# Kernel tuning notes

Measured on AMD Instinct MI355X. Metric: run time of the kernel, lower is better.

Reference implementation:

```python
import jax, jax.numpy as jnp
import numpy as np

N, E, D, H = 50000, 800000, 128, 8
DK = D // H
SQRT_DK = float(np.sqrt(DK))
LN_EPS = 1e-5


def setup_inputs() -> dict:
    key = jax.random.key(0)
    ks = jax.random.split(key, 16)
    s = 0.02
    inp = {
        "x": jax.random.normal(ks[0], (N, D), jnp.float32),
        "edge_index": jax.random.randint(ks[1], (2, E), 0, N, jnp.int32),
        "Wq": jax.random.normal(ks[2], (D, D), jnp.float32) * s,
        "bq": jnp.zeros((D,), jnp.float32),
        "Wk": jax.random.normal(ks[3], (D, D), jnp.float32) * s,
        "bk": jnp.zeros((D,), jnp.float32),
        "Wv": jax.random.normal(ks[4], (D, D), jnp.float32) * s,
        "bv": jnp.zeros((D,), jnp.float32),
        "ln_g": jnp.ones((D,), jnp.float32),
        "ln_b": jnp.zeros((D,), jnp.float32),
        "W1": jax.random.normal(ks[5], (D, 2 * D), jnp.float32) * s,
        "b1": jnp.zeros((2 * D,), jnp.float32),
        "W2": jax.random.normal(ks[6], (2 * D, D), jnp.float32) * s,
        "b2": jnp.zeros((D,), jnp.float32),
    }
    return inp


def _segment_softmax(scores, seg, num_segments):
    # scores: [E, H], seg: [E] target-node ids. Matches PyG softmax (1e-16 in denom).
    m = jax.ops.segment_max(scores, seg, num_segments=num_segments)
    ex = jnp.exp(scores - m[seg])
    den = jax.ops.segment_sum(ex, seg, num_segments=num_segments)
    return ex / (den[seg] + 1e-16)


def _forward(x, edge_index, Wq, bq, Wk, bk, Wv, bv, ln_g, ln_b, W1, b1, W2, b2):
    src, dst = edge_index[0], edge_index[1]
    n = x.shape[0]
    x_src = x[src]            # [E, D] gather
    x_dst = x[dst]            # [E, D] gather
    q = (x_dst @ Wq + bq).reshape(-1, H, DK)
    k = (x_src @ Wk + bk).reshape(-1, H, DK)
    v = (x_src @ Wv + bv).reshape(-1, H, DK)
    att = jnp.sum(q * k, axis=-1) / SQRT_DK          # [E, H]; edge_weight defaults to 1
    att = _segment_softmax(att, dst, n)              # segment softmax over dst
    msg = (v * att[..., None]).reshape(-1, D)        # [E, D]
    res = jax.ops.segment_sum(msg, dst, num_segments=n)  # scatter-add
    h = res + x
    # FFN with pre-LayerNorm, residual h + mlp(LN(h))
    mu = jnp.mean(h, axis=-1, keepdims=True)
    var = jnp.mean(jnp.square(h - mu), axis=-1, keepdims=True)
    hn = (h - mu) * jax.lax.rsqrt(var + LN_EPS) * ln_g + ln_b
    mlp = jax.nn.gelu(hn @ W1 + b1, approximate=False) @ W2 + b2
    return h + mlp


def reference(x, edge_index, Wq, bq, Wk, bk, Wv, bv, ln_g, ln_b, W1, b1, W2, b2):
    return _forward(x, edge_index, Wq, bq, Wk, bk, Wv, bv, ln_g, ln_b, W1, b1, W2, b2)
```

## Files before the change

kernel.cpp:

```cpp
#include <hip/hip_runtime.h>
#include <cmath>


typedef short v8s __attribute__((ext_vector_type(8)));
typedef float v4f __attribute__((ext_vector_type(4)));
typedef float v2f __attribute__((ext_vector_type(2)));

__device__ __forceinline__ float gelu_exact(float x) {
    return 0.5f * x * (1.0f + erff(x * 0.70710678118654752440f));
}

__device__ __forceinline__ unsigned short f2bf(float f) {
    unsigned int u = __float_as_uint(f);
    u = (u + 0x7fffu + ((u >> 16) & 1u)) >> 16;
    return (unsigned short)u;
}

__device__ __forceinline__ float2 bf2_to_f2(unsigned int u) {
    float2 r;
    r.x = __uint_as_float(u << 16);
    r.y = __uint_as_float(u & 0xffff0000u);
    return r;
}

__device__ __forceinline__ unsigned char f2fp8(float f) {
    unsigned int p = __builtin_amdgcn_cvt_pk_fp8_f32(f, f, 0, false);
    return (unsigned char)(p & 0xffu);
}

__device__ __forceinline__ void edge_accum(uint4 k4, uint4 v4, bool ok,
                                           const float2 (&qv)[8],
                                           float2 (&acc)[8], float& l) {
    v2f f;
    float d0 = 0.f, d1 = 0.f;
    f = __builtin_amdgcn_cvt_pk_f32_fp8(k4.x, false); d0 = fmaf(f[0], qv[0].x, fmaf(f[1], qv[0].y, d0));
    f = __builtin_amdgcn_cvt_pk_f32_fp8(k4.x, true);  d1 = fmaf(f[0], qv[1].x, fmaf(f[1], qv[1].y, d1));
    f = __builtin_amdgcn_cvt_pk_f32_fp8(k4.y, false); d0 = fmaf(f[0], qv[2].x, fmaf(f[1], qv[2].y, d0));
    f = __builtin_amdgcn_cvt_pk_f32_fp8(k4.y, true);  d1 = fmaf(f[0], qv[3].x, fmaf(f[1], qv[3].y, d1));
    f = __builtin_amdgcn_cvt_pk_f32_fp8(k4.z, false); d0 = fmaf(f[0], qv[4].x, fmaf(f[1], qv[4].y, d0));
    f = __builtin_amdgcn_cvt_pk_f32_fp8(k4.z, true);  d1 = fmaf(f[0], qv[5].x, fmaf(f[1], qv[5].y, d1));
    f = __builtin_amdgcn_cvt_pk_f32_fp8(k4.w, false); d0 = fmaf(f[0], qv[6].x, fmaf(f[1], qv[6].y, d0));
    f = __builtin_amdgcn_cvt_pk_f32_fp8(k4.w, true);  d1 = fmaf(f[0], qv[7].x, fmaf(f[1], qv[7].y, d1));
    float pe = ok ? __expf(d0 + d1) : 0.f;
    l += pe;
    f = __builtin_amdgcn_cvt_pk_f32_fp8(v4.x, false); acc[0].x = fmaf(pe, f[0], acc[0].x); acc[0].y = fmaf(pe, f[1], acc[0].y);
    f = __builtin_amdgcn_cvt_pk_f32_fp8(v4.x, true);  acc[1].x = fmaf(pe, f[0], acc[1].x); acc[1].y = fmaf(pe, f[1], acc[1].y);
    f = __builtin_amdgcn_cvt_pk_f32_fp8(v4.y, false); acc[2].x = fmaf(pe, f[0], acc[2].x); acc[2].y = fmaf(pe, f[1], acc[2].y);
    f = __builtin_amdgcn_cvt_pk_f32_fp8(v4.y, true);  acc[3].x = fmaf(pe, f[0], acc[3].x); acc[3].y = fmaf(pe, f[1], acc[3].y);
    f = __builtin_amdgcn_cvt_pk_f32_fp8(v4.z, false); acc[4].x = fmaf(pe, f[0], acc[4].x); acc[4].y = fmaf(pe, f[1], acc[4].y);
    f = __builtin_amdgcn_cvt_pk_f32_fp8(v4.z, true);  acc[5].x = fmaf(pe, f[0], acc[5].x); acc[5].y = fmaf(pe, f[1], acc[5].y);
    f = __builtin_amdgcn_cvt_pk_f32_fp8(v4.w, false); acc[6].x = fmaf(pe, f[0], acc[6].x); acc[6].y = fmaf(pe, f[1], acc[6].y);
    f = __builtin_amdgcn_cvt_pk_f32_fp8(v4.w, true);  acc[7].x = fmaf(pe, f[0], acc[7].x); acc[7].y = fmaf(pe, f[1], acc[7].y);
}


__global__ __launch_bounds__(256)
void prep_kernel(const float* __restrict__ Wq, const float* __restrict__ Wk,
                 const float* __restrict__ Wv, const float* __restrict__ W1,
                 const float* __restrict__ W2,
                 const float* __restrict__ bq, const float* __restrict__ bk,
                 const float* __restrict__ bv, const float* __restrict__ b1,
                 const float* __restrict__ b2,
                 unsigned short* __restrict__ wcat, unsigned short* __restrict__ w1t,
                 unsigned short* __restrict__ w2t, float* __restrict__ bcat) {
    int i = blockIdx.x * 256 + threadIdx.x;
    if (i < 49152) {
        int m = i >> 14, j = i & 16383;
        int c = j >> 7, k = j & 127;
        const float* W = (m == 0) ? Wq : (m == 1) ? Wk : Wv;
        wcat[i] = f2bf(W[k * 128 + c]);
    } else if (i < 49152 + 32768) {
        int j = i - 49152;
        int c = j >> 7, k = j & 127;
        w1t[j] = f2bf(W1[k * 256 + c]);
    } else if (i < 49152 + 65536) {
        int j = i - 49152 - 32768;
        int c = j >> 8, k = j & 255;
        w2t[j] = f2bf(W2[k * 128 + c]);
    } else if (i < 49152 + 65536 + 768) {
        int j = i - 49152 - 65536;
        float v;
        if (j < 128)      v = bq[j];
        else if (j < 256) v = bk[j - 128];
        else if (j < 384) v = bv[j - 256];
        else if (j < 640) v = b1[j - 384];
        else              v = b2[j - 640];
        bcat[j] = v;
    }
}


__global__ __launch_bounds__(256)
void scatter_kernel(const int* __restrict__ src, const int* __restrict__ dst,
                    int* __restrict__ cnt, int* __restrict__ slots, int E,
                    int nseg, int nbpr) {
    const int r = blockIdx.x & 7;
    const int b = blockIdx.x >> 3;
    const int lo = r * nseg, hi = lo + nseg;
    const int stride = nbpr * 256;
    const int E4 = E >> 2;
    for (int i = b * 256 + threadIdx.x; i < E4; i += stride) {
        int4 d4 = ((const int4*)dst)[i];
        int4 s4 = ((const int4*)src)[i];
        if (d4.x >= lo && d4.x < hi) { int p = atomicAdd(&cnt[d4.x], 1); if (p < 64) slots[(d4.x << 6) + p] = s4.x; }
        if (d4.y >= lo && d4.y < hi) { int p = atomicAdd(&cnt[d4.y], 1); if (p < 64) slots[(d4.y << 6) + p] = s4.y; }
        if (d4.z >= lo && d4.z < hi) { int p = atomicAdd(&cnt[d4.z], 1); if (p < 64) slots[(d4.z << 6) + p] = s4.z; }
        if (d4.w >= lo && d4.w < hi) { int p = atomicAdd(&cnt[d4.w], 1); if (p < 64) slots[(d4.w << 6) + p] = s4.w; }
    }
    if (b == 0) {
        for (int e = (E4 << 2) + threadIdx.x; e < E; e += 256) {
            int d = dst[e];
            if (d >= lo && d < hi) {
                int p = atomicAdd(&cnt[d], 1);
                if (p < 64) slots[(d << 6) + p] = src[e];
            }
        }
    }
}


__global__ __launch_bounds__(512)
void qkv_gemm_kernel(const float* __restrict__ A,
                     const unsigned short* __restrict__ wcat,
                     const float* __restrict__ bcat,
                     unsigned short* __restrict__ qb,
                     unsigned char* __restrict__ kvh,
                     int n_rows) {
    __shared__ unsigned short Xs[8192];

    const int t = threadIdx.x;
    const int l = t & 63;
    const int w = t >> 6;
    const int lq = l >> 4;
    const int lc = l & 15;
    const int rb = blockIdx.x * 64;

    #pragma unroll
    for (int it = 0; it < 2; ++it) {
        int idx = it * 512 + t;
        int row = idx >> 4, ch = idx & 15;
        v8s av = (v8s){0, 0, 0, 0, 0, 0, 0, 0};
        if (rb + row < n_rows) {
            const float* ap = &A[(size_t)(rb + row) * 128 + ch * 8];
            float4 f0 = *(const float4*)ap;
            float4 f1 = *(const float4*)(ap + 4);
            av[0] = (short)f2bf(f0.x); av[1] = (short)f2bf(f0.y);
            av[2] = (short)f2bf(f0.z); av[3] = (short)f2bf(f0.w);
            av[4] = (short)f2bf(f1.x); av[5] = (short)f2bf(f1.y);
            av[6] = (short)f2bf(f1.z); av[7] = (short)f2bf(f1.w);
        }
        *(v8s*)&Xs[row * 128 + ((ch ^ (row & 7)) * 8)] = av;
    }
    __syncthreads();

    v8s a[4][4];
    #pragma unroll
    for (int c = 0; c < 4; ++c)
        #pragma unroll
        for (int i = 0; i < 4; ++i)
            a[c][i] = *(const v8s*)&Xs[(i * 16 + lc) * 128 +
                                       (((c * 4 + lq) ^ (lc & 7)) * 8)];

    const int col = w * 16 + lc;
    #pragma unroll
    for (int y = 0; y < 3; ++y) {
        const unsigned short* Bt = wcat + y * 16384;
        v8s bf[4];
        #pragma unroll
        for (int c = 0; c < 4; ++c)
            bf[c] = *(const v8s*)&Bt[(size_t)col * 128 + c * 32 + lq * 8];

        v4f acc[4];
        #pragma unroll
        for (int i = 0; i < 4; ++i) acc[i] = (v4f){0.f, 0.f, 0.f, 0.f};
        #pragma unroll
        for (int c = 0; c < 4; ++c)
            #pragma unroll
            for (int i = 0; i < 4; ++i)
                acc[i] = __builtin_amdgcn_mfma_f32_16x16x32_bf16(a[c][i], bf[c], acc[i], 0, 0, 0);

        float bi = bcat[y * 128 + col];
        #pragma unroll
        for (int i = 0; i < 4; ++i) {
            #pragma unroll
            for (int reg = 0; reg < 4; ++reg) {
                int rr = rb + i * 16 + lq * 4 + reg;
                if (rr >= n_rows) continue;
                float vv = acc[i][reg] + bi;
                if (y == 0)
                    qb[(size_t)rr * 128 + col] = f2bf(vv);
                else
                    kvh[(size_t)rr * 256 + w * 32 + lc + (y == 2 ? 16 : 0)] = f2fp8(vv);
            }
        }
    }
}


__global__ __launch_bounds__(512)
void ffn_fused_kernel(const unsigned short* __restrict__ hnb,
                      const unsigned short* __restrict__ w1t,
                      const unsigned short* __restrict__ w2t,
                      const float* __restrict__ bcat,
                      const float* __restrict__ hb,
                      float* __restrict__ out, int n_rows) {
    __shared__ unsigned short As[8192];
    __shared__ unsigned short H1[16384];

    const int t = threadIdx.x;
    const int l = t & 63;
    const int w = t >> 6;
    const int lq = l >> 4;
    const int lc = l & 15;
    const int rb = blockIdx.x * 64;

    #pragma unroll
    for (int it = 0; it < 2; ++it) {
        int idx = it * 512 + t;
        int row = idx >> 4, ch = idx & 15;
        v8s av = (v8s){0, 0, 0, 0, 0, 0, 0, 0};
        if (rb + row < n_rows)
            av = *(const v8s*)&hnb[(size_t)(rb + row) * 128 + ch * 8];
        *(v8s*)&As[row * 128 + ((ch ^ (row & 7)) * 8)] = av;
    }

    v8s b1f[2][4];
    #pragma unroll
    for (int j = 0; j < 2; ++j)
        #pragma unroll
        for (int c = 0; c < 4; ++c) {
            int colm = w * 32 + j * 16 + lc;
            b1f[j][c] = *(const v8s*)&w1t[(size_t)colm * 128 + c * 32 + lq * 8];
        }
    __syncthreads();

    v4f acc1[4][2];
    #pragma unroll
    for (int i = 0; i < 4; ++i)
        #pragma unroll
        for (int j = 0; j < 2; ++j)
            acc1[i][j] = (v4f){0.f, 0.f, 0.f, 0.f};

    #pragma unroll
    for (int c = 0; c < 4; ++c) {
        v8s a[4];
        #pragma unroll
        for (int i = 0; i < 4; ++i)
            a[i] = *(const v8s*)&As[(i * 16 + lc) * 128 +
                                    (((c * 4 + lq) ^ (lc & 7)) * 8)];
        #pragma unroll
        for (int i = 0; i < 4; ++i)
            #pragma unroll
            for (int j = 0; j < 2; ++j)
                acc1[i][j] = __builtin_amdgcn_mfma_f32_16x16x32_bf16(a[i], b1f[j][c], acc1[i][j], 0, 0, 0);
    }

    #pragma unroll
    for (int j = 0; j < 2; ++j) {
        int colm = w * 32 + j * 16 + lc;
        float bi = bcat[384 + colm];
        int ch = colm >> 3;
        #pragma unroll
        for (int i = 0; i < 4; ++i) {
            #pragma unroll
            for (int reg = 0; reg < 4; ++reg) {
                int r = i * 16 + lq * 4 + reg;
                float vv = gelu_exact(acc1[i][j][reg] + bi);
                H1[r * 256 + ((ch ^ (r & 7)) * 8) + (colm & 7)] = f2bf(vv);
            }
        }
    }

    const int col = w * 16 + lc;
    v8s b2f[8];
    #pragma unroll
    for (int c = 0; c < 8; ++c)
        b2f[c] = *(const v8s*)&w2t[(size_t)col * 256 + c * 32 + lq * 8];
    __syncthreads();

    v4f acc2[4];
    #pragma unroll
    for (int i = 0; i < 4; ++i) acc2[i] = (v4f){0.f, 0.f, 0.f, 0.f};

    #pragma unroll
    for (int c = 0; c < 8; ++c) {
        #pragma unroll
        for (int i = 0; i < 4; ++i) {
            v8s a = *(const v8s*)&H1[(i * 16 + lc) * 256 +
                                     (((c * 4 + lq) ^ (lc & 7)) * 8)];
            acc2[i] = __builtin_amdgcn_mfma_f32_16x16x32_bf16(a, b2f[c], acc2[i], 0, 0, 0);
        }
    }

    float bi2 = bcat[640 + col];
    #pragma unroll
    for (int i = 0; i < 4; ++i) {
        #pragma unroll
        for (int reg = 0; reg < 4; ++reg) {
            int rr = rb + i * 16 + lq * 4 + reg;
            if (rr >= n_rows) continue;
            out[(size_t)rr * 128 + col] =
                acc2[i][reg] + bi2 + hb[(size_t)rr * 128 + col];
        }
    }
}


__global__ __launch_bounds__(256)
void attn_ln_kernel(const unsigned short* __restrict__ q,
                    const unsigned char* __restrict__ kvh,
                    const float* __restrict__ x,
                    const int* __restrict__ cnt, const int* __restrict__ slots,
                    const float* __restrict__ ln_g, const float* __restrict__ ln_b,
                    float* __restrict__ hb, unsigned short* __restrict__ hnb, int n) {
    const int wave = threadIdx.x >> 6;
    const int lane = threadIdx.x & 63;
    const int node = blockIdx.x * 4 + wave;
    if (node >= n) return;
    const int head = lane & 7;
    const int slot = lane >> 3;

    const unsigned int* qp = (const unsigned int*)&q[(size_t)node * 128 + head * 16];
    float2 qv[8];
    #pragma unroll
    for (int i = 0; i < 8; ++i) {
        qv[i] = bf2_to_f2(qp[i]);
        qv[i].x *= 0.25f;
        qv[i].y *= 0.25f;
    }

    const int deg = min(cnt[node], 64);

    float l = 0.f;
    float2 acc[8];
    #pragma unroll
    for (int i = 0; i < 8; ++i) acc[i] = make_float2(0.f, 0.f);

    if (deg > 0) {
        const int base = node << 6;
        const int dlast = deg - 1;
        for (int j = 0; j < deg; j += 16) {
            int ea = j + slot;
            int eb = ea + 8;
            bool oka = ea < deg;
            bool okb = eb < deg;
            int sa = slots[base + (oka ? ea : dlast)];
            int sb = slots[base + (okb ? eb : dlast)];
            const uint4* kpa = (const uint4*)&kvh[(size_t)sa * 256 + head * 32];
            const uint4* kpb = (const uint4*)&kvh[(size_t)sb * 256 + head * 32];
            uint4 ka  = kpa[0];
            uint4 va4 = kpa[1];
            uint4 kb  = kpb[0];
            uint4 vb4 = kpb[1];
            edge_accum(ka, va4, oka, qv, acc, l);
            edge_accum(kb, vb4, okb, qv, acc, l);
        }
    }

    const bool b0 = (slot & 1) != 0, b1 = (slot & 2) != 0, b2 = (slot & 4) != 0;
    float2 k0[4];
    #pragma unroll
    for (int j = 0; j < 4; ++j) {
        float2 snd = b0 ? acc[2 * j] : acc[2 * j + 1];
        float2 kp  = b0 ? acc[2 * j + 1] : acc[2 * j];
        snd.x = __shfl_xor(snd.x, 8, 64);
        snd.y = __shfl_xor(snd.y, 8, 64);
        k0[j] = make_float2(kp.x + snd.x, kp.y + snd.y);
    }
    float2 k1[2];
    #pragma unroll
    for (int j = 0; j < 2; ++j) {
        float2 snd = b1 ? k0[2 * j] : k0[2 * j + 1];
        float2 kp  = b1 ? k0[2 * j + 1] : k0[2 * j];
        snd.x = __shfl_xor(snd.x, 16, 64);
        snd.y = __shfl_xor(snd.y, 16, 64);
        k1[j] = make_float2(kp.x + snd.x, kp.y + snd.y);
    }
    {
        float2 snd = b2 ? k1[0] : k1[1];
        float2 kp  = b2 ? k1[1] : k1[0];
        snd.x = __shfl_xor(snd.x, 32, 64);
        snd.y = __shfl_xor(snd.y, 32, 64);
        k1[0] = make_float2(kp.x + snd.x, kp.y + snd.y);
    }
    float2 o = k1[0];

    l += __shfl_xor(l, 8, 64);
    l += __shfl_xor(l, 16, 64);
    l += __shfl_xor(l, 32, 64);

    float inv = 1.f / (l + 1e-16f);

    const int d = head * 16 + slot * 2;
    float2 xv = *(const float2*)&x[(size_t)node * 128 + d];
    float2 hv = make_float2(o.x * inv + xv.x, o.y * inv + xv.y);
    *(float2*)&hb[(size_t)node * 128 + d] = hv;

    float s  = hv.x + hv.y;
    float s2 = hv.x * hv.x + hv.y * hv.y;
    #pragma unroll
    for (int off = 1; off < 64; off <<= 1) {
        s  += __shfl_xor(s, off, 64);
        s2 += __shfl_xor(s2, off, 64);
    }
    float mu  = s * (1.f / 128.f);
    float var = s2 * (1.f / 128.f) - mu * mu;
    float rstd = rsqrtf(var + 1e-5f);
    float2 gv = *(const float2*)&ln_g[d];
    float2 bv = *(const float2*)&ln_b[d];
    ushort2 ob;
    ob.x = f2bf((hv.x - mu) * rstd * gv.x + bv.x);
    ob.y = f2bf((hv.y - mu) * rstd * gv.y + bv.y);
    *(ushort2*)&hnb[(size_t)node * 128 + d] = ob;
}


extern "C" void kernel_launch(void* const* d_in, const int* in_sizes, int n_in,
                              void* d_out, int out_size, void* d_ws, size_t ws_size,
                              hipStream_t stream) {
    const float* x    = (const float*)d_in[0];
    const int*   ei   = (const int*)d_in[1];
    const float* Wq   = (const float*)d_in[2];
    const float* bq   = (const float*)d_in[3];
    const float* Wk   = (const float*)d_in[4];
    const float* bk   = (const float*)d_in[5];
    const float* Wv   = (const float*)d_in[6];
    const float* bv   = (const float*)d_in[7];
    const float* ln_g = (const float*)d_in[8];
    const float* ln_b = (const float*)d_in[9];
    const float* W1   = (const float*)d_in[10];
    const float* b1   = (const float*)d_in[11];
    const float* W2   = (const float*)d_in[12];
    const float* b2   = (const float*)d_in[13];
    float* out = (float*)d_out;

    const int D = 128;
    const int N = in_sizes[0] / D;
    const int E = in_sizes[1] / 2;
    const int* src = ei;
    const int* dst = ei + E;

    const size_t ND = (size_t)N * D;
    unsigned short* qb  = (unsigned short*)d_ws;
    unsigned char*  kvh = (unsigned char*)(qb + ND);
    float*          hb  = (float*)(kvh + (size_t)N * 256);
    unsigned short* hnb = (unsigned short*)(hb + ND);
    unsigned short* wcat = hnb + ND;
    unsigned short* w1t  = wcat + 49152;
    unsigned short* w2t  = w1t + 32768;
    float* bcat = (float*)(w2t + 32768);
    int* cnt   = (int*)(bcat + 768);
    int* slots = cnt + N;

    const int nprep = (49152 + 65536 + 768 + 255) / 256;
    const int rt64  = (N + 63) / 64;
    const int nseg  = (N + 7) / 8;
    const int nbpr  = 196;
    const int nscat = 8 * nbpr;

    hipMemsetAsync(cnt, 0, sizeof(int) * N, stream);
    prep_kernel<<<nprep, 256, 0, stream>>>(Wq, Wk, Wv, W1, W2,
                                           bq, bk, bv, b1, b2,
                                           wcat, w1t, w2t, bcat);
    scatter_kernel<<<nscat, 256, 0, stream>>>(src, dst, cnt, slots, E,
                                              nseg, nbpr);
    qkv_gemm_kernel<<<rt64, 512, 0, stream>>>(x, wcat, bcat, qb, kvh, N);
    attn_ln_kernel<<<(N + 3) / 4, 256, 0, stream>>>(qb, kvh, x, cnt, slots,
                                                    ln_g, ln_b, hb, hnb, N);
    ffn_fused_kernel<<<rt64, 512, 0, stream>>>(hnb, w1t, w2t, bcat, hb, out, N);
}
```

Before: 260.7 us.

## Fuse attention+LayerNorm into FFN kernel, writing normalized rows directly to LDS

Merges the per-node attention/LayerNorm kernel into the FFN kernel: each of the 8 waves in a 512-thread block processes 8 nodes serially, computing attention, residual and LayerNorm, and stores the bf16 normalized row straight into the swizzled LDS tile used by the first MFMA GEMM. This removes the hnb global buffer round trip and one kernel launch. In exchange, the gather-heavy attention phase now runs with far fewer blocks (64 nodes per block), serially per wave, which can reduce latency hiding. The block also holds large LDS allocations while doing irregular gathers.

```diff
diff --git a/kernel.cpp b/kernel.cpp
--- a/kernel.cpp
+++ b/kernel.cpp
@@ -30,7 +30,7 @@
 
 __device__ __forceinline__ void edge_accum(uint4 k4, uint4 v4, bool ok,
                                            const float2 (&qv)[8],
-                                           float2 (&acc)[8], float& l) {
+                                           float2 (&acc)[8], float& sml) {
     v2f f;
     float d0 = 0.f, d1 = 0.f;
     f = __builtin_amdgcn_cvt_pk_f32_fp8(k4.x, false); d0 = fmaf(f[0], qv[0].x, fmaf(f[1], qv[0].y, d0));
@@ -42,7 +42,7 @@
     f = __builtin_amdgcn_cvt_pk_f32_fp8(k4.w, false); d0 = fmaf(f[0], qv[6].x, fmaf(f[1], qv[6].y, d0));
     f = __builtin_amdgcn_cvt_pk_f32_fp8(k4.w, true);  d1 = fmaf(f[0], qv[7].x, fmaf(f[1], qv[7].y, d1));
     float pe = ok ? __expf(d0 + d1) : 0.f;
-    l += pe;
+    sml += pe;
     f = __builtin_amdgcn_cvt_pk_f32_fp8(v4.x, false); acc[0].x = fmaf(pe, f[0], acc[0].x); acc[0].y = fmaf(pe, f[1], acc[0].y);
     f = __builtin_amdgcn_cvt_pk_f32_fp8(v4.x, true);  acc[1].x = fmaf(pe, f[0], acc[1].x); acc[1].y = fmaf(pe, f[1], acc[1].y);
     f = __builtin_amdgcn_cvt_pk_f32_fp8(v4.y, false); acc[2].x = fmaf(pe, f[0], acc[2].x); acc[2].y = fmaf(pe, f[1], acc[2].y);
@@ -198,12 +198,15 @@
 
 
 __global__ __launch_bounds__(512)
-void ffn_fused_kernel(const unsigned short* __restrict__ hnb,
-                      const unsigned short* __restrict__ w1t,
-                      const unsigned short* __restrict__ w2t,
-                      const float* __restrict__ bcat,
-                      const float* __restrict__ hb,
-                      float* __restrict__ out, int n_rows) {
+void attn_ffn_kernel(const unsigned short* __restrict__ q,
+                     const unsigned char* __restrict__ kvh,
+                     const float* __restrict__ x,
+                     const int* __restrict__ cnt, const int* __restrict__ slots,
+                     const float* __restrict__ ln_g, const float* __restrict__ ln_b,
+                     const unsigned short* __restrict__ w1t,
+                     const unsigned short* __restrict__ w2t,
+                     const float* __restrict__ bcat,
+                     float* __restrict__ hb, float* __restrict__ out, int n) {
     __shared__ unsigned short As[8192];
     __shared__ unsigned short H1[16384];
 
@@ -213,15 +216,112 @@
     const int lq = l >> 4;
     const int lc = l & 15;
     const int rb = blockIdx.x * 64;
-
-    #pragma unroll
-    for (int it = 0; it < 2; ++it) {
-        int idx = it * 512 + t;
-        int row = idx >> 4, ch = idx & 15;
-        v8s av = (v8s){0, 0, 0, 0, 0, 0, 0, 0};
-        if (rb + row < n_rows)
-            av = *(const v8s*)&hnb[(size_t)(rb + row) * 128 + ch * 8];
-        *(v8s*)&As[row * 128 + ((ch ^ (row & 7)) * 8)] = av;
+    const int head = l & 7;
+    const int slot = l >> 3;
+    const int d = head * 16 + slot * 2;
+
+    const float2 gv = *(const float2*)&ln_g[d];
+    const float2 bv = *(const float2*)&ln_b[d];
+
+    for (int n8 = 0; n8 < 8; ++n8) {
+        const int row = w * 8 + n8;
+        const int node = rb + row;
+        const int aoff = row * 128 + (((d >> 3) ^ n8) * 8) + (d & 7);
+        if (node >= n) {
+            ushort2 z; z.x = 0; z.y = 0;
+            *(ushort2*)&As[aoff] = z;
+            continue;
+        }
+
+        const unsigned int* qp = (const unsigned int*)&q[(size_t)node * 128 + head * 16];
+        float2 qv[8];
+        #pragma unroll
+        for (int i = 0; i < 8; ++i) {
+            qv[i] = bf2_to_f2(qp[i]);
+            qv[i].x *= 0.25f;
+            qv[i].y *= 0.25f;
+        }
+
+        const int deg = min(cnt[node], 64);
+
+        float sml = 0.f;
+        float2 acc[8];
+        #pragma unroll
+        for (int i = 0; i < 8; ++i) acc[i] = make_float2(0.f, 0.f);
+
+        if (deg > 0) {
+            const int base = node << 6;
+            const int dlast = deg - 1;
+            for (int j = 0; j < deg; j += 16) {
+                int ea = j + slot;
+                int eb = ea + 8;
+                bool oka = ea < deg;
+                bool okb = eb < deg;
+                int sa = slots[base + (oka ? ea : dlast)];
+                int sb = slots[base + (okb ? eb : dlast)];
+                const uint4* kpa = (const uint4*)&kvh[(size_t)sa * 256 + head * 32];
+                const uint4* kpb = (const uint4*)&kvh[(size_t)sb * 256 + head * 32];
+                uint4 ka  = kpa[0];
+                uint4 va4 = kpa[1];
+                uint4 kb  = kpb[0];
+                uint4 vb4 = kpb[1];
+                edge_accum(ka, va4, oka, qv, acc, sml);
+                edge_accum(kb, vb4, okb, qv, acc, sml);
+            }
+        }
+
+        const bool s0 = (slot & 1) != 0, s1 = (slot & 2) != 0, s2 = (slot & 4) != 0;
+        float2 k0[4];
+        #pragma unroll
+        for (int j = 0; j < 4; ++j) {
+            float2 snd = s0 ? acc[2 * j] : acc[2 * j + 1];
+            float2 kp  = s0 ? acc[2 * j + 1] : acc[2 * j];
+            snd.x = __shfl_xor(snd.x, 8, 64);
+            snd.y = __shfl_xor(snd.y, 8, 64);
+            k0[j] = make_float2(kp.x + snd.x, kp.y + snd.y);
+        }
+        float2 k1[2];
+        #pragma unroll
+        for (int j = 0; j < 2; ++j) {
+            float2 snd = s1 ? k0[2 * j] : k0[2 * j + 1];
+            float2 kp  = s1 ? k0[2 * j + 1] : k0[2 * j];
+            snd.x = __shfl_xor(snd.x, 16, 64);
+            snd.y = __shfl_xor(snd.y, 16, 64);
+            k1[j] = make_float2(kp.x + snd.x, kp.y + snd.y);
+        }
+        {
+            float2 snd = s2 ? k1[0] : k1[1];
+            float2 kp  = s2 ? k1[1] : k1[0];
+            snd.x = __shfl_xor(snd.x, 32, 64);
+            snd.y = __shfl_xor(snd.y, 32, 64);
+            k1[0] = make_float2(kp.x + snd.x, kp.y + snd.y);
+        }
+        float2 o = k1[0];
+
+        sml += __shfl_xor(sml, 8, 64);
+        sml += __shfl_xor(sml, 16, 64);
+        sml += __shfl_xor(sml, 32, 64);
+
+        float inv = 1.f / (sml + 1e-16f);
+
+        float2 xv = *(const float2*)&x[(size_t)node * 128 + d];
+        float2 hv = make_float2(o.x * inv + xv.x, o.y * inv + xv.y);
+        *(float2*)&hb[(size_t)node * 128 + d] = hv;
+
+        float s  = hv.x + hv.y;
+        float s2v = hv.x * hv.x + hv.y * hv.y;
+        #pragma unroll
+        for (int off = 1; off < 64; off <<= 1) {
+            s   += __shfl_xor(s, off, 64);
+            s2v += __shfl_xor(s2v, off, 64);
+        }
+        float mu  = s * (1.f / 128.f);
+        float var = s2v * (1.f / 128.f) - mu * mu;
+        float rstd = rsqrtf(var + 1e-5f);
+        ushort2 ob;
+        ob.x = f2bf((hv.x - mu) * rstd * gv.x + bv.x);
+        ob.y = f2bf((hv.y - mu) * rstd * gv.y + bv.y);
+        *(ushort2*)&As[aoff] = ob;
     }
 
     v8s b1f[2][4];
@@ -232,6 +332,7 @@
             int colm = w * 32 + j * 16 + lc;
             b1f[j][c] = *(const v8s*)&w1t[(size_t)colm * 128 + c * 32 + lq * 8];
         }
+    __threadfence_block();
     __syncthreads();
 
     v4f acc1[4][2];
@@ -298,120 +399,11 @@
         #pragma unroll
         for (int reg = 0; reg < 4; ++reg) {
             int rr = rb + i * 16 + lq * 4 + reg;
-            if (rr >= n_rows) continue;
+            if (rr >= n) continue;
             out[(size_t)rr * 128 + col] =
                 acc2[i][reg] + bi2 + hb[(size_t)rr * 128 + col];
         }
     }
-}
-
-
-__global__ __launch_bounds__(256)
-void attn_ln_kernel(const unsigned short* __restrict__ q,
-                    const unsigned char* __restrict__ kvh,
-                    const float* __restrict__ x,
-                    const int* __restrict__ cnt, const int* __restrict__ slots,
-                    const float* __restrict__ ln_g, const float* __restrict__ ln_b,
-                    float* __restrict__ hb, unsigned short* __restrict__ hnb, int n) {
-    const int wave = threadIdx.x >> 6;
-    const int lane = threadIdx.x & 63;
-    const int node = blockIdx.x * 4 + wave;
-    if (node >= n) return;
-    const int head = lane & 7;
-    const int slot = lane >> 3;
-
-    const unsigned int* qp = (const unsigned int*)&q[(size_t)node * 128 + head * 16];
-    float2 qv[8];
-    #pragma unroll
-    for (int i = 0; i < 8; ++i) {
-        qv[i] = bf2_to_f2(qp[i]);
-        qv[i].x *= 0.25f;
-        qv[i].y *= 0.25f;
-    }
-
-    const int deg = min(cnt[node], 64);
-
-    float l = 0.f;
-    float2 acc[8];
-    #pragma unroll
-    for (int i = 0; i < 8; ++i) acc[i] = make_float2(0.f, 0.f);
-
-    if (deg > 0) {
-        const int base = node << 6;
-        const int dlast = deg - 1;
-        for (int j = 0; j < deg; j += 16) {
-            int ea = j + slot;
-            int eb = ea + 8;
-            bool oka = ea < deg;
-            bool okb = eb < deg;
-            int sa = slots[base + (oka ? ea : dlast)];
-            int sb = slots[base + (okb ? eb : dlast)];
-            const uint4* kpa = (const uint4*)&kvh[(size_t)sa * 256 + head * 32];
-            const uint4* kpb = (const uint4*)&kvh[(size_t)sb * 256 + head * 32];
-            uint4 ka  = kpa[0];
-            uint4 va4 = kpa[1];
-            uint4 kb  = kpb[0];
-            uint4 vb4 = kpb[1];
-            edge_accum(ka, va4, oka, qv, acc, l);
-            edge_accum(kb, vb4, okb, qv, acc, l);
-        }
-    }
-
-    const bool b0 = (slot & 1) != 0, b1 = (slot & 2) != 0, b2 = (slot & 4) != 0;
-    float2 k0[4];
-    #pragma unroll
-    for (int j = 0; j < 4; ++j) {
-        float2 snd = b0 ? acc[2 * j] : acc[2 * j + 1];
-        float2 kp  = b0 ? acc[2 * j + 1] : acc[2 * j];
-        snd.x = __shfl_xor(snd.x, 8, 64);
-        snd.y = __shfl_xor(snd.y, 8, 64);
-        k0[j] = make_float2(kp.x + snd.x, kp.y + snd.y);
-    }
-    float2 k1[2];
-    #pragma unroll
-    for (int j = 0; j < 2; ++j) {
-        float2 snd = b1 ? k0[2 * j] : k0[2 * j + 1];
-        float2 kp  = b1 ? k0[2 * j + 1] : k0[2 * j];
-        snd.x = __shfl_xor(snd.x, 16, 64);
-        snd.y = __shfl_xor(snd.y, 16, 64);
-        k1[j] = make_float2(kp.x + snd.x, kp.y + snd.y);
-    }
-    {
-        float2 snd = b2 ? k1[0] : k1[1];
-        float2 kp  = b2 ? k1[1] : k1[0];
-        snd.x = __shfl_xor(snd.x, 32, 64);
-        snd.y = __shfl_xor(snd.y, 32, 64);
-        k1[0] = make_float2(kp.x + snd.x, kp.y + snd.y);
-    }
-    float2 o = k1[0];
-
-    l += __shfl_xor(l, 8, 64);
-    l += __shfl_xor(l, 16, 64);
-    l += __shfl_xor(l, 32, 64);
-
-    float inv = 1.f / (l + 1e-16f);
-
-    const int d = head * 16 + slot * 2;
-    float2 xv = *(const float2*)&x[(size_t)node * 128 + d];
-    float2 hv = make_float2(o.x * inv + xv.x, o.y * inv + xv.y);
-    *(float2*)&hb[(size_t)node * 128 + d] = hv;
-
-    float s  = hv.x + hv.y;
-    float s2 = hv.x * hv.x + hv.y * hv.y;
-    #pragma unroll
-    for (int off = 1; off < 64; off <<= 1) {
-        s  += __shfl_xor(s, off, 64);
-        s2 += __shfl_xor(s2, off, 64);
-    }
-    float mu  = s * (1.f / 128.f);
-    float var = s2 * (1.f / 128.f) - mu * mu;
-    float rstd = rsqrtf(var + 1e-5f);
-    float2 gv = *(const float2*)&ln_g[d];
-    float2 bv = *(const float2*)&ln_b[d];
-    ushort2 ob;
-    ob.x = f2bf((hv.x - mu) * rstd * gv.x + bv.x);
-    ob.y = f2bf((hv.y - mu) * rstd * gv.y + bv.y);
-    *(ushort2*)&hnb[(size_t)node * 128 + d] = ob;
 }
 
 
@@ -444,8 +436,7 @@
     unsigned short* qb  = (unsigned short*)d_ws;
     unsigned char*  kvh = (unsigned char*)(qb + ND);
     float*          hb  = (float*)(kvh + (size_t)N * 256);
-    unsigned short* hnb = (unsigned short*)(hb + ND);
-    unsigned short* wcat = hnb + ND;
+    unsigned short* wcat = (unsigned short*)(hb + ND);
     unsigned short* w1t  = wcat + 49152;
     unsigned short* w2t  = w1t + 32768;
     float* bcat = (float*)(w2t + 32768);
@@ -465,7 +456,7 @@
     scatter_kernel<<<nscat, 256, 0, stream>>>(src, dst, cnt, slots, E,
                                               nseg, nbpr);
     qkv_gemm_kernel<<<rt64, 512, 0, stream>>>(x, wcat, bcat, qb, kvh, N);
-    attn_ln_kernel<<<(N + 3) / 4, 256, 0, stream>>>(qb, kvh, x, cnt, slots,
-                                                    ln_g, ln_b, hb, hnb, N);
-    ffn_fused_kernel<<<rt64, 512, 0, stream>>>(hnb, w1t, w2t, bcat, hb, out, N);
-}
+    attn_ffn_kernel<<<rt64, 512, 0, stream>>>(qb, kvh, x, cnt, slots,
+                                              ln_g, ln_b, w1t, w2t, bcat,
+                                              hb, out, N);
+}
```

Result: no change. 262.8 us (+0.8%).
